# Optimization experiments

Measured on AMD Instinct MI355X. Metric: run time of the kernel, lower is better.

Reference implementation:

```python
import jax, jax.numpy as jnp
import numpy as np

HID = 2048
N_HEADS = 16
N_KV = 16
HEAD_DIM = HID // N_HEADS
N_EXP = 8
TOP_K = 2
MOE_I = 1408
SH_I = 5632
EPS = 1e-6
ROPE_THETA = 1e6


def _rms(x, w):
    v = jnp.mean(jnp.square(x), axis=-1, keepdims=True)
    return (x * jax.lax.rsqrt(v + EPS)) * w


def _rope(q, k):
    # q, k: [B, S, H, D]
    S, D = q.shape[1], q.shape[-1]
    inv = 1.0 / (ROPE_THETA ** (jnp.arange(0, D, 2, dtype=jnp.float32) / D))
    freqs = jnp.arange(S, dtype=jnp.float32)[:, None] * inv[None, :]   # [S, D/2]
    emb = jnp.concatenate([freqs, freqs], axis=-1)                      # [S, D]
    cos = jnp.cos(emb)[None, :, None, :]
    sin = jnp.sin(emb)[None, :, None, :]
    def rot(t):
        t1, t2 = t[..., : D // 2], t[..., D // 2:]
        return jnp.concatenate([-t2, t1], axis=-1)
    return q * cos + rot(q) * sin, k * cos + rot(k) * sin


def setup_inputs() -> dict:
    key = jax.random.key(0)
    ks = jax.random.split(key, 20)
    s = 0.02
    d = {
        "x": jax.random.normal(ks[0], (2, 1024, HID), jnp.float32),
        "w_ln1": jnp.ones((HID,), jnp.float32),
        "wq": jax.random.normal(ks[1], (HID, N_HEADS * HEAD_DIM), jnp.float32) * s,
        "bq": jnp.zeros((N_HEADS * HEAD_DIM,), jnp.float32),
        "wk": jax.random.normal(ks[2], (HID, N_KV * HEAD_DIM), jnp.float32) * s,
        "bk": jnp.zeros((N_KV * HEAD_DIM,), jnp.float32),
        "wv": jax.random.normal(ks[3], (HID, N_KV * HEAD_DIM), jnp.float32) * s,
        "bv": jnp.zeros((N_KV * HEAD_DIM,), jnp.float32),
        "wo": jax.random.normal(ks[4], (N_HEADS * HEAD_DIM, HID), jnp.float32) * s,
        "w_ln2": jnp.ones((HID,), jnp.float32),
        "w_router": jax.random.normal(ks[5], (HID, N_EXP), jnp.float32) * s,
        "w_gate_e": jax.random.normal(ks[6], (N_EXP, HID, MOE_I), jnp.float32) * s,
        "w_up_e": jax.random.normal(ks[7], (N_EXP, HID, MOE_I), jnp.float32) * s,
        "w_down_e": jax.random.normal(ks[8], (N_EXP, MOE_I, HID), jnp.float32) * s,
        "w_sh_gate": jax.random.normal(ks[9], (HID, SH_I), jnp.float32) * s,
        "w_sh_up": jax.random.normal(ks[10], (HID, SH_I), jnp.float32) * s,
        "w_sh_down": jax.random.normal(ks[11], (SH_I, HID), jnp.float32) * s,
        "w_sh_eg": jax.random.normal(ks[12], (HID, 1), jnp.float32) * s,
    }
    return d


def reference(x, w_ln1, wq, bq, wk, bk, wv, bv, wo, w_ln2, w_router,
              w_gate_e, w_up_e, w_down_e, w_sh_gate, w_sh_up, w_sh_down, w_sh_eg):
    B, S, H = x.shape
    # ---- self-attention (pre-norm) ----
    h = _rms(x, w_ln1)
    q = (h @ wq + bq).reshape(B, S, N_HEADS, HEAD_DIM)
    k = (h @ wk + bk).reshape(B, S, N_KV, HEAD_DIM)
    v = (h @ wv + bv).reshape(B, S, N_KV, HEAD_DIM)
    q, k = _rope(q, k)
    rep = N_HEADS // N_KV
    if rep > 1:
        k = jnp.repeat(k, rep, axis=2)
        v = jnp.repeat(v, rep, axis=2)
    scores = jnp.einsum("bqhd,bkhd->bhqk", q, k) * (HEAD_DIM ** -0.5)
    causal = jnp.tril(jnp.ones((S, S), bool))
    scores = jnp.where(causal[None, None], scores, jnp.finfo(scores.dtype).min)
    attn = jax.nn.softmax(scores, axis=-1)
    ctx = jnp.einsum("bhqk,bkhd->bqhd", attn, v).reshape(B, S, N_HEADS * HEAD_DIM)
    x = x + ctx @ wo

    # ---- sparse MoE FFN (pre-norm) ----
    h = _rms(x, w_ln2).reshape(B * S, H)                     # [T, H]
    logits = h @ w_router                                     # [T, E]
    probs = jax.nn.softmax(logits, axis=-1)
    top_w, top_i = jax.lax.top_k(probs, TOP_K)               # norm_topk_prob=False
    combine = jnp.sum(jax.nn.one_hot(top_i, N_EXP, dtype=h.dtype)
                      * top_w[..., None], axis=1)            # [T, E]
    # dense per-expert compute combined with routing weights (same math as
    # the sorted grouped-GEMM dispatch in Qwen2MoeMLPStack)
    g = jnp.einsum("th,ehi->eti", h, w_gate_e)               # [E, T, I]
    u = jnp.einsum("th,ehi->eti", h, w_up_e)
    y = jnp.einsum("eti,eih->eth", jax.nn.silu(g) * u, w_down_e)
    routed = jnp.einsum("eth,te->th", y, combine)            # [T, H]
    # shared expert with sigmoid gate
    sh = (jax.nn.silu(h @ w_sh_gate) * (h @ w_sh_up)) @ w_sh_down
    sh = sh * jax.nn.sigmoid(h @ w_sh_eg)
    x = x + (routed + sh).reshape(B, S, H)
    return x
```

## Files before the change

kernel.cpp:

```cpp
#include <hip/hip_runtime.h>
#include <hip/hip_bf16.h>
#include <math.h>

#define TOKENS 2048
#define HIDDEN 2048
#define NH 16
#define HD 128
#define SEQ 1024
#define MOE_I 1408
#define SH_I 5632
#define K3 6144
#define MAXROWS 5120

typedef __hip_bfloat16 bf16;
typedef short bf16x8 __attribute__((ext_vector_type(8)));
typedef short bf16x4 __attribute__((ext_vector_type(4)));
typedef float f32x4 __attribute__((ext_vector_type(4)));

__device__ __forceinline__ float b2f(bf16 x) { return __bfloat162float(x); }
__device__ __forceinline__ bf16 f2b(float x) { return __float2bfloat16(x); }
__device__ __forceinline__ void split2(float v, short& hi, short& lo) {
    bf16 h = f2b(v);
    bf16 l = f2b(v - b2f(h));
    hi = __builtin_bit_cast(short, h); lo = __builtin_bit_cast(short, l);
}

__device__ __forceinline__ void load_lds16(const void* g, void* l) {
    __builtin_amdgcn_global_load_lds(
        (const __attribute__((address_space(1))) unsigned int*)g,
        (__attribute__((address_space(3))) unsigned int*)l, 16, 0, 0);
}

__global__ __launch_bounds__(256) void rmsnorm3_k(
    const float* __restrict__ x, const float* __restrict__ w, bf16* __restrict__ out)
{
    const int row = blockIdx.x, tid = threadIdx.x;
    const float4* xr = (const float4*)(x + (size_t)row * HIDDEN);
    float4 v1 = xr[tid], v2 = xr[tid + 256];
    float ss = v1.x*v1.x + v1.y*v1.y + v1.z*v1.z + v1.w*v1.w
             + v2.x*v2.x + v2.y*v2.y + v2.z*v2.z + v2.w*v2.w;
    #pragma unroll
    for (int off = 1; off < 64; off <<= 1) ss += __shfl_xor(ss, off);
    __shared__ float ps[4];
    if ((tid & 63) == 0) ps[tid >> 6] = ss;
    __syncthreads();
    float tot = ps[0] + ps[1] + ps[2] + ps[3];
    float r = rsqrtf(tot * (1.0f / HIDDEN) + 1e-6f);
    bf16* o = out + (size_t)row * 4096;
    float vv[8] = {v1.x, v1.y, v1.z, v1.w, v2.x, v2.y, v2.z, v2.w};
    int idx[8]  = {tid*4, tid*4+1, tid*4+2, tid*4+3,
                   1024+tid*4, 1024+tid*4+1, 1024+tid*4+2, 1024+tid*4+3};
    #pragma unroll
    for (int u = 0; u < 8; u++) {
        short hi, lo; split2(vv[u] * r * w[idx[u]], hi, lo);
        o[idx[u]]        = __builtin_bit_cast(bf16, hi);
        o[2048 + idx[u]] = __builtin_bit_cast(bf16, lo);
    }
}

__global__ __launch_bounds__(256) void transpose_wz(
    const float* __restrict__ W, bf16* __restrict__ Wt, int K, int N,
    int nOff, long zsrc, long zdst)
{
    __shared__ float t[32][33];
    W  += (size_t)blockIdx.z * zsrc;
    Wt += (size_t)blockIdx.z * zdst;
    const int n0 = blockIdx.x * 32, k0 = blockIdx.y * 32;
    const int tx = threadIdx.x & 31, ty = threadIdx.x >> 5;
    #pragma unroll
    for (int i = 0; i < 4; i++)
        t[ty + i*8][tx] = W[(size_t)(k0 + ty + i*8) * N + n0 + tx];
    __syncthreads();
    #pragma unroll
    for (int i = 0; i < 4; i++)
        Wt[(size_t)(nOff + n0 + ty + i*8) * K + k0 + tx] = f2b(t[tx][ty + i*8]);
}

__global__ __launch_bounds__(256) void transpose_w3(
    const float* __restrict__ W, bf16* __restrict__ Wt2, int K, int N, int nOff)
{
    __shared__ float t[32][33];
    const int n0 = blockIdx.x * 32, k0 = blockIdx.y * 32;
    const int tx = threadIdx.x & 31, ty = threadIdx.x >> 5;
    #pragma unroll
    for (int i = 0; i < 4; i++)
        t[ty + i*8][tx] = W[(size_t)(k0 + ty + i*8) * N + n0 + tx];
    __syncthreads();
    #pragma unroll
    for (int i = 0; i < 4; i++) {
        float v = t[tx][ty + i*8];
        short hi, lo; split2(v, hi, lo);
        bf16* o = Wt2 + (size_t)(nOff + n0 + ty + i*8) * (2*K) + k0 + tx;
        o[0] = __builtin_bit_cast(bf16, hi);
        o[K] = __builtin_bit_cast(bf16, lo);
    }
}

__global__ __launch_bounds__(256) void gemm_bt(
    const bf16* __restrict__ A, const bf16* __restrict__ Bt,
    float* __restrict__ Cf, bf16* __restrict__ Cb, const float* __restrict__ bias,
    int M, int N, int K, int ldA, int ldB, int ldC, long zCstride, int limb3, int epi)
{
    __shared__ __align__(16) bf16 As[128 * 32];
    __shared__ __align__(16) bf16 Bs[128 * 32];
    const int tid = threadIdx.x;
    const int lane = tid & 63, wid = tid >> 6;
    const int l16 = lane & 15, lh = lane >> 4;
    const int wr = wid >> 1, wc = wid & 1;
    const int m0 = blockIdx.x * 128, n0 = blockIdx.y * 128;
    const int f = tid * 8;
    const int r0 = f >> 5, c0 = f & 31;
    const int koff = blockIdx.z * K;

    f32x4 acc[4][4];
    #pragma unroll
    for (int m = 0; m < 4; m++)
        #pragma unroll
        for (int n = 0; n < 4; n++) acc[m][n] = (f32x4){0.f, 0.f, 0.f, 0.f};

    const bf16* Ag0 = A + (size_t)(m0 + r0) * ldA + c0;
    const bf16* Ag1 = Ag0 + (size_t)64 * ldA;
    const bf16* Bg0 = Bt + (size_t)(n0 + r0) * ldB + c0;
    const bf16* Bg1 = Bg0 + (size_t)64 * ldB;

    for (int k0 = 0; k0 < K; k0 += 32) {
        const int kcat = koff + k0;
        int ka = kcat, kb = kcat;
        if (limb3) {
            ka = (kcat >= 4096) ? kcat - 4096 : kcat;
            kb = (kcat >= 2048) ? kcat - 2048 : kcat;
        }
        __syncthreads();
        load_lds16(Ag0 + ka, As + f);
        load_lds16(Ag1 + ka, As + f + 2048);
        load_lds16(Bg0 + kb, Bs + f);
        load_lds16(Bg1 + kb, Bs + f + 2048);
        __syncthreads();
        bf16x8 a[4], b[4];
        #pragma unroll
        for (int m = 0; m < 4; m++)
            a[m] = *(const bf16x8*)&As[(wr*64 + m*16 + l16) * 32 + lh*8];
        #pragma unroll
        for (int n = 0; n < 4; n++)
            b[n] = *(const bf16x8*)&Bs[(wc*64 + n*16 + l16) * 32 + lh*8];
        #pragma unroll
        for (int m = 0; m < 4; m++)
            #pragma unroll
            for (int n = 0; n < 4; n++)
                acc[m][n] = __builtin_amdgcn_mfma_f32_16x16x32_bf16(a[m], b[n], acc[m][n], 0, 0, 0);
    }

    float* Cz = Cf + (size_t)blockIdx.z * zCstride;
    #pragma unroll
    for (int m = 0; m < 4; m++) {
        const int grow_base = m0 + wr*64 + m*16 + lh*4;
        #pragma unroll
        for (int n = 0; n < 4; n++) {
            const int gcol = n0 + wc*64 + n*16 + l16;
            #pragma unroll
            for (int j = 0; j < 4; j++) {
                const size_t o = (size_t)(grow_base + j) * ldC + gcol;
                const float v = acc[m][n][j];
                if (epi == 0)      Cb[o] = f2b(v);
                else if (epi == 4) Cz[o] = v;
                else               Cf[o] = v + bias[gcol];
            }
        }
    }
}

__global__ __launch_bounds__(256) void gemm_gu(
    const bf16* __restrict__ A, const bf16* __restrict__ BtAll,
    const int* __restrict__ offc, const int* __restrict__ perm,
    bf16* __restrict__ C)
{
    const int e = blockIdx.z;
    const int off = offc[8 + e];
    const int padCnt = offc[9 + e] - off;
    const int m0 = blockIdx.x * 128;
    if (m0 >= padCnt) return;
    __shared__ __align__(16) bf16 As[128 * 32];
    __shared__ __align__(16) bf16 Bs[128 * 32];
    const int tid = threadIdx.x;
    const int lane = tid & 63, wid = tid >> 6;
    const int l16 = lane & 15, lh = lane >> 4;
    const int wr = wid >> 1, wc = wid & 1;
    const int n0 = blockIdx.y * 128;
    const int f = tid * 8;
    const int r0 = f >> 5, c0 = f & 31;
    const bf16* Bt = BtAll + (size_t)e * 2816 * 2048;

    int t0 = perm[off + m0 + r0];      if (t0 < 0) t0 = 0;
    int t1 = perm[off + m0 + r0 + 64]; if (t1 < 0) t1 = 0;

    f32x4 acc[4][4];
    #pragma unroll
    for (int m = 0; m < 4; m++)
        #pragma unroll
        for (int n = 0; n < 4; n++) acc[m][n] = (f32x4){0.f, 0.f, 0.f, 0.f};

    const bf16* Ag0 = A + (size_t)t0 * 2048 + c0;
    const bf16* Ag1 = A + (size_t)t1 * 2048 + c0;
    const bf16* Bg0 = Bt + (size_t)(n0 + r0) * 2048 + c0;
    const bf16* Bg1 = Bg0 + (size_t)64 * 2048;

    for (int k0 = 0; k0 < 2048; k0 += 32) {
        __syncthreads();
        load_lds16(Ag0 + k0, As + f);
        load_lds16(Ag1 + k0, As + f + 2048);
        load_lds16(Bg0 + k0, Bs + f);
        load_lds16(Bg1 + k0, Bs + f + 2048);
        __syncthreads();
        bf16x8 a[4], b[4];
        #pragma unroll
        for (int m = 0; m < 4; m++)
            a[m] = *(const bf16x8*)&As[(wr*64 + m*16 + l16) * 32 + lh*8];
        #pragma unroll
        for (int n = 0; n < 4; n++)
            b[n] = *(const bf16x8*)&Bs[(wc*64 + n*16 + l16) * 32 + lh*8];
        #pragma unroll
        for (int m = 0; m < 4; m++)
            #pragma unroll
            for (int n = 0; n < 4; n++)
                acc[m][n] = __builtin_amdgcn_mfma_f32_16x16x32_bf16(a[m], b[n], acc[m][n], 0, 0, 0);
    }

    #pragma unroll
    for (int m = 0; m < 4; m++) {
        const int grow_base = m0 + wr*64 + m*16 + lh*4;
        #pragma unroll
        for (int n = 0; n < 4; n++) {
            const int gcol = n0 + wc*64 + n*16 + l16;
            #pragma unroll
            for (int j = 0; j < 4; j++)
                C[(size_t)(off + grow_base + j) * 2816 + gcol] = f2b(acc[m][n][j]);
        }
    }
}

__global__ __launch_bounds__(256) void gemm_down(
    const bf16* __restrict__ A, const bf16* __restrict__ BtAll,
    const int* __restrict__ offc, bf16* __restrict__ Y)
{
    const int e = blockIdx.z;
    const int off = offc[8 + e];
    const int padCnt = offc[9 + e] - off;
    const int m0 = blockIdx.x * 128;
    if (m0 >= padCnt) return;
    __shared__ __align__(16) bf16 As[128 * 32];
    __shared__ __align__(16) bf16 Bs[128 * 32];
    const int tid = threadIdx.x;
    const int lane = tid & 63, wid = tid >> 6;
    const int l16 = lane & 15, lh = lane >> 4;
    const int wr = wid >> 1, wc = wid & 1;
    const int n0 = blockIdx.y * 128;
    const int f = tid * 8;
    const int r0 = f >> 5, c0 = f & 31;
    const bf16* Bt = BtAll + (size_t)e * 2048 * 1408;

    f32x4 acc[4][4];
    #pragma unroll
    for (int m = 0; m < 4; m++)
        #pragma unroll
        for (int n = 0; n < 4; n++) acc[m][n] = (f32x4){0.f, 0.f, 0.f, 0.f};

    const bf16* Ag0 = A + (size_t)(off + m0 + r0) * 1408 + c0;
    const bf16* Ag1 = Ag0 + (size_t)64 * 1408;
    const bf16* Bg0 = Bt + (size_t)(n0 + r0) * 1408 + c0;
    const bf16* Bg1 = Bg0 + (size_t)64 * 1408;

    for (int k0 = 0; k0 < 1408; k0 += 32) {
        __syncthreads();
        load_lds16(Ag0 + k0, As + f);
        load_lds16(Ag1 + k0, As + f + 2048);
        load_lds16(Bg0 + k0, Bs + f);
        load_lds16(Bg1 + k0, Bs + f + 2048);
        __syncthreads();
        bf16x8 a[4], b[4];
        #pragma unroll
        for (int m = 0; m < 4; m++)
            a[m] = *(const bf16x8*)&As[(wr*64 + m*16 + l16) * 32 + lh*8];
        #pragma unroll
        for (int n = 0; n < 4; n++)
            b[n] = *(const bf16x8*)&Bs[(wc*64 + n*16 + l16) * 32 + lh*8];
        #pragma unroll
        for (int m = 0; m < 4; m++)
            #pragma unroll
            for (int n = 0; n < 4; n++)
                acc[m][n] = __builtin_amdgcn_mfma_f32_16x16x32_bf16(a[m], b[n], acc[m][n], 0, 0, 0);
    }

    #pragma unroll
    for (int m = 0; m < 4; m++) {
        const int grow_base = m0 + wr*64 + m*16 + lh*4;
        #pragma unroll
        for (int n = 0; n < 4; n++) {
            const int gcol = n0 + wc*64 + n*16 + l16;
            #pragma unroll
            for (int j = 0; j < 4; j++)
                Y[(size_t)(off + grow_base + j) * 2048 + gcol] = f2b(acc[m][n][j]);
        }
    }
}

__global__ void rope_f32_k(float* __restrict__ qkv)
{
    const int idx = blockIdx.x * 256 + threadIdx.x;
    const int d  = idx & 63;
    const int hh = (idx >> 6) & 15;
    const size_t base = (size_t)(idx >> 10) * 6144 + hh * HD;
    const int s = (idx >> 10) & 1023;
    const float fr = (float)s * powf(1.0e6f, -(float)d * (1.0f / 64.0f));
    float c, sn;
    sincosf(fr, &sn, &c);
    float q0 = qkv[base + d], q1 = qkv[base + d + 64];
    qkv[base + d]      = q0 * c - q1 * sn;
    qkv[base + d + 64] = q1 * c + q0 * sn;
    float k0 = qkv[base + 2048 + d], k1 = qkv[base + 2048 + d + 64];
    qkv[base + 2048 + d]      = k0 * c - k1 * sn;
    qkv[base + 2048 + d + 64] = k1 * c + k0 * sn;
}

__global__ __launch_bounds__(256) void transpose_v3_k(
    const float* __restrict__ qkv, bf16* __restrict__ vth, bf16* __restrict__ vtl)
{
    __shared__ float t[32][33];
    const int s0 = blockIdx.x * 32, d0 = blockIdx.y * 32;
    const int bh = blockIdx.z, b = bh >> 4, h = bh & 15;
    const int tx = threadIdx.x & 31, ty = threadIdx.x >> 5;
    const float* vb = qkv + ((size_t)b * SEQ) * 6144 + 4096 + h * HD;
    #pragma unroll
    for (int i = 0; i < 4; i++)
        t[ty + i*8][tx] = vb[(size_t)(s0 + ty + i*8) * 6144 + d0 + tx];
    __syncthreads();
    const size_t ob = ((size_t)bh * HD) * SEQ;
    #pragma unroll
    for (int i = 0; i < 4; i++) {
        float val = t[tx][ty + i*8];
        short hi, lo; split2(val, hi, lo);
        const size_t o = ob + (size_t)(d0 + ty + i*8) * SEQ + s0 + tx;
        vth[o] = __builtin_bit_cast(bf16, hi);
        vtl[o] = __builtin_bit_cast(bf16, lo);
    }
}

__global__ __launch_bounds__(256) void attn3_k(
    const float* __restrict__ qkv,
    const bf16* __restrict__ vth, const bf16* __restrict__ vtl,
    bf16* __restrict__ ctx2)
{
    __shared__ __align__(16) bf16 Ksh[32 * 128], Ksl[32 * 128];
    __shared__ __align__(16) bf16 Vth[128 * 32], Vtl[128 * 32];
    __shared__ __align__(16) bf16 Ph[4][16 * 32], Pl[4][16 * 32];
    const int tid = threadIdx.x, lane = tid & 63, wid = tid >> 6;
    const int l16 = lane & 15, lh = lane >> 4;
    const int bh = blockIdx.y, b = bh >> 4, h = bh & 15;
    const int qbase = blockIdx.x * 64;
    const int qw = qbase + wid * 16;
    const float* qp = qkv + ((size_t)b * SEQ) * 6144 + h * HD;
    const float* kp = qkv + ((size_t)b * SEQ) * 6144 + 2048 + h * HD;
    const bf16* vph = vth + ((size_t)bh * HD) * SEQ;
    const bf16* vpl = vtl + ((size_t)bh * HD) * SEQ;

    bf16x8 aqh[4], aql[4];
    #pragma unroll
    for (int c = 0; c < 4; c++) {
        const float* qrow = qp + (size_t)(qw + l16) * 6144 + c*32 + lh*8;
        #pragma unroll
        for (int u = 0; u < 8; u++) {
            short hi, lo; split2(qrow[u], hi, lo);
            aqh[c][u] = hi; aql[c][u] = lo;
        }
    }

    f32x4 o[8];
    #pragma unroll
    for (int n = 0; n < 8; n++) o[n] = (f32x4){0.f, 0.f, 0.f, 0.f};
    float mj[4], lj[4];
    #pragma unroll
    for (int j = 0; j < 4; j++) { mj[j] = -1e30f; lj[j] = 0.f; }

    const int f = tid * 8;
    const int kr = tid >> 3, kc = (tid & 7) * 16;
    const int kt_end = qbase / 32 + 2;
    for (int kt = 0; kt < kt_end; ++kt) {
        const int kv0 = kt * 32;
        __syncthreads();
        {
            const float* krow = kp + (size_t)(kv0 + kr) * 6144 + kc;
            #pragma unroll
            for (int u = 0; u < 4; u++) {
                float4 kv4 = *(const float4*)(krow + u*4);
                short h0, l0, h1, l1, h2s, l2s, h3, l3;
                split2(kv4.x, h0, l0); split2(kv4.y, h1, l1);
                split2(kv4.z, h2s, l2s); split2(kv4.w, h3, l3);
                bf16x4 h4, l4;
                h4[0] = h0; h4[1] = h1; h4[2] = h2s; h4[3] = h3;
                l4[0] = l0; l4[1] = l1; l4[2] = l2s; l4[3] = l3;
                *(bf16x4*)&Ksh[kr*128 + kc + u*4] = h4;
                *(bf16x4*)&Ksl[kr*128 + kc + u*4] = l4;
            }
        }
        load_lds16(vph + (size_t)(f >> 5) * SEQ + kv0 + (f & 31), Vth + f);
        load_lds16(vph + (size_t)((f >> 5) + 64) * SEQ + kv0 + (f & 31), Vth + f + 2048);
        load_lds16(vpl + (size_t)(f >> 5) * SEQ + kv0 + (f & 31), Vtl + f);
        load_lds16(vpl + (size_t)((f >> 5) + 64) * SEQ + kv0 + (f & 31), Vtl + f + 2048);
        __syncthreads();

        f32x4 s0a = (f32x4){0.f,0.f,0.f,0.f}, s1a = (f32x4){0.f,0.f,0.f,0.f};
        #pragma unroll
        for (int c = 0; c < 4; c++) {
            bf16x8 bk0h = *(const bf16x8*)&Ksh[(l16) * 128 + c*32 + lh*8];
            bf16x8 bk0l = *(const bf16x8*)&Ksl[(l16) * 128 + c*32 + lh*8];
            bf16x8 bk1h = *(const bf16x8*)&Ksh[(l16 + 16) * 128 + c*32 + lh*8];
            bf16x8 bk1l = *(const bf16x8*)&Ksl[(l16 + 16) * 128 + c*32 + lh*8];
            s0a = __builtin_amdgcn_mfma_f32_16x16x32_bf16(aqh[c], bk0h, s0a, 0, 0, 0);
            s0a = __builtin_amdgcn_mfma_f32_16x16x32_bf16(aql[c], bk0h, s0a, 0, 0, 0);
            s0a = __builtin_amdgcn_mfma_f32_16x16x32_bf16(aqh[c], bk0l, s0a, 0, 0, 0);
            s1a = __builtin_amdgcn_mfma_f32_16x16x32_bf16(aqh[c], bk1h, s1a, 0, 0, 0);
            s1a = __builtin_amdgcn_mfma_f32_16x16x32_bf16(aql[c], bk1h, s1a, 0, 0, 0);
            s1a = __builtin_amdgcn_mfma_f32_16x16x32_bf16(aqh[c], bk1l, s1a, 0, 0, 0);
        }
        const float scale = 0.08838834764831845f;
        #pragma unroll
        for (int j = 0; j < 4; j++) {
            const int qrow = qw + lh*4 + j;
            float s0 = s0a[j] * scale, s1 = s1a[j] * scale;
            if (kv0 + l16 > qrow)      s0 = -1e30f;
            if (kv0 + l16 + 16 > qrow) s1 = -1e30f;
            float mx = fmaxf(s0, s1);
            #pragma unroll
            for (int off = 1; off < 16; off <<= 1) mx = fmaxf(mx, __shfl_xor(mx, off, 16));
            const float nm = fmaxf(mj[j], mx);
            const float al = __expf(mj[j] - nm);
            const float p0 = __expf(s0 - nm), p1 = __expf(s1 - nm);
            float rs = p0 + p1;
            #pragma unroll
            for (int off = 1; off < 16; off <<= 1) rs += __shfl_xor(rs, off, 16);
            lj[j] = lj[j] * al + rs;
            mj[j] = nm;
            #pragma unroll
            for (int n = 0; n < 8; n++) o[n][j] *= al;
            short h0, l0, h1, l1;
            split2(p0, h0, l0); split2(p1, h1, l1);
            Ph[wid][(lh*4 + j) * 32 + l16]      = __builtin_bit_cast(bf16, h0);
            Pl[wid][(lh*4 + j) * 32 + l16]      = __builtin_bit_cast(bf16, l0);
            Ph[wid][(lh*4 + j) * 32 + l16 + 16] = __builtin_bit_cast(bf16, h1);
            Pl[wid][(lh*4 + j) * 32 + l16 + 16] = __builtin_bit_cast(bf16, l1);
        }
        __syncthreads();
        const bf16x8 aph = *(const bf16x8*)&Ph[wid][l16 * 32 + lh*8];
        const bf16x8 apl = *(const bf16x8*)&Pl[wid][l16 * 32 + lh*8];
        #pragma unroll
        for (int n = 0; n < 8; n++) {
            bf16x8 bvh = *(const bf16x8*)&Vth[(n*16 + l16) * 32 + lh*8];
            bf16x8 bvl = *(const bf16x8*)&Vtl[(n*16 + l16) * 32 + lh*8];
            o[n] = __builtin_amdgcn_mfma_f32_16x16x32_bf16(aph, bvh, o[n], 0, 0, 0);
            o[n] = __builtin_amdgcn_mfma_f32_16x16x32_bf16(apl, bvh, o[n], 0, 0, 0);
            o[n] = __builtin_amdgcn_mfma_f32_16x16x32_bf16(aph, bvl, o[n], 0, 0, 0);
        }
    }

    float inv[4];
    #pragma unroll
    for (int j = 0; j < 4; j++) inv[j] = 1.0f / lj[j];
    #pragma unroll
    for (int n = 0; n < 8; n++)
        #pragma unroll
        for (int j = 0; j < 4; j++) {
            const float v = o[n][j] * inv[j];
            short hi, lo; split2(v, hi, lo);
            const size_t base = ((size_t)b * SEQ + (qw + lh*4 + j)) * 4096 + h * HD + n*16 + l16;
            ctx2[base]        = __builtin_bit_cast(bf16, hi);
            ctx2[base + 2048] = __builtin_bit_cast(bf16, lo);
        }
}

__global__ __launch_bounds__(256) void combine_rms_k(
    const float* __restrict__ x, const float* __restrict__ xp,
    const float* __restrict__ w, float* __restrict__ x1, bf16* __restrict__ h2)
{
    const int row = blockIdx.x, tid = threadIdx.x;
    const size_t rb = (size_t)row * HIDDEN;
    const long zs = (long)TOKENS * HIDDEN;
    float4 v[2];
    #pragma unroll
    for (int u = 0; u < 2; u++) {
        const int i = tid + u * 256;
        float4 a  = ((const float4*)(x + rb))[i];
        float4 p0 = ((const float4*)(xp + rb))[i];
        float4 p1 = ((const float4*)(xp + zs + rb))[i];
        float4 p2 = ((const float4*)(xp + 2*zs + rb))[i];
        v[u].x = a.x + p0.x + p1.x + p2.x;
        v[u].y = a.y + p0.y + p1.y + p2.y;
        v[u].z = a.z + p0.z + p1.z + p2.z;
        v[u].w = a.w + p0.w + p1.w + p2.w;
        ((float4*)(x1 + rb))[i] = v[u];
    }
    float ss = v[0].x*v[0].x + v[0].y*v[0].y + v[0].z*v[0].z + v[0].w*v[0].w
             + v[1].x*v[1].x + v[1].y*v[1].y + v[1].z*v[1].z + v[1].w*v[1].w;
    #pragma unroll
    for (int off = 1; off < 64; off <<= 1) ss += __shfl_xor(ss, off);
    __shared__ float ps[4];
    if ((tid & 63) == 0) ps[tid >> 6] = ss;
    __syncthreads();
    float tot = ps[0] + ps[1] + ps[2] + ps[3];
    float r = rsqrtf(tot * (1.0f / HIDDEN) + 1e-6f);
    #pragma unroll
    for (int u = 0; u < 2; u++) {
        const int i = (tid + u * 256) * 4;
        h2[rb + i]     = f2b(v[u].x * r * w[i]);
        h2[rb + i + 1] = f2b(v[u].y * r * w[i+1]);
        h2[rb + i + 2] = f2b(v[u].z * r * w[i+2]);
        h2[rb + i + 3] = f2b(v[u].w * r * w[i+3]);
    }
}

__global__ __launch_bounds__(256) void router_k(
    const float* __restrict__ x1, const float* __restrict__ wln,
    const float* __restrict__ wr, const float* __restrict__ weg,
    float* __restrict__ combine, float* __restrict__ sigeg)
{
    const int wid = threadIdx.x >> 6, lane = threadIdx.x & 63;
    const int t = blockIdx.x * 4 + wid;
    const float* xr = x1 + (size_t)t * HIDDEN;
    float ss = 0.f;
    for (int c = lane; c < HIDDEN; c += 64) { const float v = xr[c]; ss += v * v; }
    #pragma unroll
    for (int off = 1; off < 64; off <<= 1) ss += __shfl_xor(ss, off);
    const float r = rsqrtf(ss * (1.0f / HIDDEN) + 1e-6f);

    float acc[9];
    #pragma unroll
    for (int e = 0; e < 9; e++) acc[e] = 0.f;
    for (int c = lane; c < HIDDEN; c += 64) {
        const float hv = xr[c] * r * wln[c];
        const float* wrow = wr + (size_t)c * 8;
        #pragma unroll
        for (int e = 0; e < 8; e++) acc[e] += hv * wrow[e];
        acc[8] += hv * weg[c];
    }
    #pragma unroll
    for (int e = 0; e < 9; e++)
        #pragma unroll
        for (int off = 1; off < 64; off <<= 1) acc[e] += __shfl_xor(acc[e], off);
    float mx = acc[0];
    #pragma unroll
    for (int e = 1; e < 8; e++) mx = fmaxf(mx, acc[e]);
    float p[8], s = 0.f;
    #pragma unroll
    for (int e = 0; e < 8; e++) { p[e] = expf(acc[e] - mx); s += p[e]; }
    const float invs = 1.0f / s;
    #pragma unroll
    for (int e = 0; e < 8; e++) p[e] *= invs;
    int i1 = 0;
    #pragma unroll
    for (int e = 1; e < 8; e++) if (p[e] > p[i1]) i1 = e;
    int i2 = (i1 == 0) ? 1 : 0;
    #pragma unroll
    for (int e = 0; e < 8; e++) if (e != i1 && p[e] > p[i2]) i2 = e;
    if (lane < 8) combine[(size_t)t * 8 + lane] = (lane == i1 || lane == i2) ? p[lane] : 0.f;
    if (lane == 0) sigeg[t] = 1.0f / (1.0f + expf(-acc[8]));
}

__global__ __launch_bounds__(256) void count_fill_k(
    const float* __restrict__ comb, int* __restrict__ offc, int* __restrict__ perm,
    float* __restrict__ scale, int* __restrict__ inv)
{
    __shared__ int cnt[8], off[9], fil[8];
    const int tid = threadIdx.x;
    if (tid < 8) { cnt[tid] = 0; fil[tid] = 0; }
    __syncthreads();
    for (int t = tid; t < TOKENS; t += 256)
        #pragma unroll
        for (int e = 0; e < 8; e++)
            if (comb[(size_t)t * 8 + e] > 0.f) atomicAdd(&cnt[e], 1);
    __syncthreads();
    if (tid == 0) {
        off[0] = 0;
        for (int e = 0; e < 8; e++) off[e+1] = off[e] + ((cnt[e] + 127) & ~127);
    }
    __syncthreads();
    for (int i = tid; i < MAXROWS; i += 256) { perm[i] = -1; scale[i] = 0.f; }
    __syncthreads();
    for (int t = tid; t < TOKENS; t += 256) {
        int j = 0;
        #pragma unroll
        for (int e = 0; e < 8; e++) {
            const float c = comb[(size_t)t * 8 + e];
            if (c > 0.f) {
                int s = atomicAdd(&fil[e], 1);
                int slot = off[e] + s;
                perm[slot] = t;
                scale[slot] = c;
                inv[t * 2 + j] = slot;
                j++;
            }
        }
    }
    __syncthreads();
    if (tid < 9) offc[8 + tid] = off[tid];
}

__global__ void silu_k(const bf16* __restrict__ g, bf16* __restrict__ a,
                       const float* __restrict__ rowScale,
                       int I, int ldg, int rowsConst, const int* __restrict__ rowsPtr)
{
    const int idx = (blockIdx.x * 256 + threadIdx.x) * 4;
    const int rows = rowsPtr ? *rowsPtr : rowsConst;
    const int row = idx / I;
    if (row >= rows) return;
    const int col = idx - row * I;
    const float s = rowScale[row];
    const bf16* gr = g + (size_t)row * ldg + col;
    bf16* ar = a + (size_t)row * I + col;
    #pragma unroll
    for (int c = 0; c < 4; c++) {
        const float gv = b2f(gr[c]), uv = b2f(gr[I + c]);
        ar[c] = f2b(s * gv / (1.0f + __expf(-gv)) * uv);
    }
}

__global__ void final_k(const float* __restrict__ x1, const bf16* __restrict__ y,
                        const int* __restrict__ inv, const float* __restrict__ ysh,
                        float* __restrict__ out)
{
    const int i = blockIdx.x * 256 + threadIdx.x;
    const int t = i >> 9;
    const int col = (i & 511) * 4;
    const int s0 = inv[t*2], s1 = inv[t*2 + 1];
    const long zs = (long)TOKENS * HIDDEN;
    float4 a  = ((const float4*)x1)[i];
    float4 h0 = ((const float4*)ysh)[i];
    float4 h1 = ((const float4*)(ysh + zs))[i];
    const bf16* y0 = y + (size_t)s0 * 2048 + col;
    const bf16* y1 = y + (size_t)s1 * 2048 + col;
    float4 r;
    r.x = a.x + h0.x + h1.x + b2f(y0[0]) + b2f(y1[0]);
    r.y = a.y + h0.y + h1.y + b2f(y0[1]) + b2f(y1[1]);
    r.z = a.z + h0.z + h1.z + b2f(y0[2]) + b2f(y1[2]);
    r.w = a.w + h0.w + h1.w + b2f(y0[3]) + b2f(y1[3]);
    ((float4*)out)[i] = r;
}

extern "C" void kernel_launch(void* const* d_in, const int* in_sizes, int n_in,
                              void* d_out, int out_size, void* d_ws, size_t ws_size,
                              hipStream_t stream)
{
    const float* x     = (const float*)d_in[0];
    const float* w_ln1 = (const float*)d_in[1];
    const float* wq    = (const float*)d_in[2];
    const float* bq    = (const float*)d_in[3];
    const float* wk    = (const float*)d_in[4];
    const float* bk    = (const float*)d_in[5];
    const float* wv    = (const float*)d_in[6];
    const float* bv    = (const float*)d_in[7];
    const float* wo    = (const float*)d_in[8];
    const float* w_ln2 = (const float*)d_in[9];
    const float* w_rt  = (const float*)d_in[10];
    const float* w_ge  = (const float*)d_in[11];
    const float* w_ue  = (const float*)d_in[12];
    const float* w_de  = (const float*)d_in[13];
    const float* w_sg  = (const float*)d_in[14];
    const float* w_su  = (const float*)d_in[15];
    const float* w_sd  = (const float*)d_in[16];
    const float* w_eg  = (const float*)d_in[17];
    float* out = (float*)d_out;
    (void)in_sizes; (void)n_in; (void)out_size; (void)ws_size;

    char* ws = (char*)d_ws;
    float* x1    = (float*)(ws + 0);
    bf16*  h2    = (bf16*)(ws + 16777216);
    float* comb  = (float*)(ws + 25165824);
    float* seg   = (float*)(ws + 25231360);
    int*   offc  = (int*)(ws + 25239552);
    float* scale = (float*)(ws + 25243648);
    int*   perm  = (int*)(ws + 25276416);
    int*   inv   = (int*)(ws + 25297920);
    float* bqkv  = (float*)(ws + 25314304);
    const size_t S = 25341952;
    bf16*  hcat  = (bf16*)(ws + S);
    bf16*  wtqkv = (bf16*)(ws + S + 16777216);
    float* qkvf  = (float*)(ws + S + 67108864);
    bf16*  vth   = (bf16*)(ws + S);
    bf16*  vtl   = (bf16*)(ws + S + 8388608);
    bf16*  ctx2  = (bf16*)(ws + S + 16777216);
    bf16*  wt3o  = (bf16*)(ws + S + 33554432);
    float* xp    = (float*)(ws + S + 50331648);
    bf16*  wtgu  = (bf16*)(ws + S);
    bf16*  gb    = (bf16*)(ws + S + 92274688);
    bf16*  ab    = (bf16*)(ws + S);
    bf16*  wtd   = (bf16*)(ws + S + 14417920);
    bf16*  ymoe  = (bf16*)(ws + S + 60555264);
    bf16*  wtshgu = (bf16*)(ws + S);
    bf16*  gsh    = (bf16*)(ws + S + 81526784);
    bf16*  ash    = (bf16*)(ws + S);
    bf16*  wtshd  = (bf16*)(ws + S + 23068672);
    float* ysh    = (float*)(ws + S + 81526784);

    rmsnorm3_k<<<TOKENS, 256, 0, stream>>>(x, w_ln1, hcat);
    (void)hipMemcpyAsync(bqkv,        bq, 8192, hipMemcpyDeviceToDevice, stream);
    (void)hipMemcpyAsync(bqkv + 2048, bk, 8192, hipMemcpyDeviceToDevice, stream);
    (void)hipMemcpyAsync(bqkv + 4096, bv, 8192, hipMemcpyDeviceToDevice, stream);

    transpose_w3<<<dim3(64, 64), 256, 0, stream>>>(wq, wtqkv, HIDDEN, HIDDEN, 0);
    transpose_w3<<<dim3(64, 64), 256, 0, stream>>>(wk, wtqkv, HIDDEN, HIDDEN, 2048);
    transpose_w3<<<dim3(64, 64), 256, 0, stream>>>(wv, wtqkv, HIDDEN, HIDDEN, 4096);
    gemm_bt<<<dim3(16, 48, 1), 256, 0, stream>>>(hcat, wtqkv, qkvf, nullptr, bqkv,
                                                 TOKENS, 6144, K3, 4096, 4096, 6144, 0, 1, 5);

    rope_f32_k<<<8192, 256, 0, stream>>>(qkvf);
    transpose_v3_k<<<dim3(32, 4, 32), 256, 0, stream>>>(qkvf, vth, vtl);
    attn3_k<<<dim3(16, 32), 256, 0, stream>>>(qkvf, vth, vtl, ctx2);

    transpose_w3<<<dim3(64, 64), 256, 0, stream>>>(wo, wt3o, HIDDEN, HIDDEN, 0);
    gemm_bt<<<dim3(16, 16, 3), 256, 0, stream>>>(ctx2, wt3o, xp, nullptr, nullptr,
                                                 TOKENS, HIDDEN, 2048, 4096, 4096, 2048,
                                                 (long)TOKENS * HIDDEN, 1, 4);
    combine_rms_k<<<TOKENS, 256, 0, stream>>>(x, xp, w_ln2, x1, h2);

    router_k<<<TOKENS / 4, 256, 0, stream>>>(x1, w_ln2, w_rt, w_eg, comb, seg);
    count_fill_k<<<1, 256, 0, stream>>>(comb, offc, perm, scale, inv);

    transpose_wz<<<dim3(44, 64, 8), 256, 0, stream>>>(w_ge, wtgu, HIDDEN, MOE_I, 0,
                                                      (long)HIDDEN*MOE_I, (long)2816*HIDDEN);
    transpose_wz<<<dim3(44, 64, 8), 256, 0, stream>>>(w_ue, wtgu, HIDDEN, MOE_I, MOE_I,
                                                      (long)HIDDEN*MOE_I, (long)2816*HIDDEN);
    gemm_gu<<<dim3(MAXROWS/128, 22, 8), 256, 0, stream>>>(h2, wtgu, offc, perm, gb);
    silu_k<<<(MAXROWS * MOE_I) / 1024, 256, 0, stream>>>(gb, ab, scale, MOE_I, 2816, 0, offc + 16);
    transpose_wz<<<dim3(64, 44, 8), 256, 0, stream>>>(w_de, wtd, MOE_I, HIDDEN, 0,
                                                      (long)MOE_I*HIDDEN, (long)HIDDEN*MOE_I);
    gemm_down<<<dim3(MAXROWS/128, 16, 8), 256, 0, stream>>>(ab, wtd, offc, ymoe);

    transpose_wz<<<dim3(176, 64, 1), 256, 0, stream>>>(w_sg, wtshgu, HIDDEN, SH_I, 0, 0, 0);
    transpose_wz<<<dim3(176, 64, 1), 256, 0, stream>>>(w_su, wtshgu, HIDDEN, SH_I, SH_I, 0, 0);
    gemm_bt<<<dim3(16, 88, 1), 256, 0, stream>>>(h2, wtshgu, nullptr, gsh, nullptr,
                                                 TOKENS, 2*SH_I, HIDDEN, HIDDEN, HIDDEN, 2*SH_I, 0, 0, 0);
    silu_k<<<(TOKENS * SH_I) / 1024, 256, 0, stream>>>(gsh, ash, seg, SH_I, 2*SH_I, TOKENS, nullptr);
    transpose_wz<<<dim3(64, 176, 1), 256, 0, stream>>>(w_sd, wtshd, SH_I, HIDDEN, 0, 0, 0);
    gemm_bt<<<dim3(16, 16, 2), 256, 0, stream>>>(ash, wtshd, ysh, nullptr, nullptr,
                                                 TOKENS, HIDDEN, SH_I/2, SH_I, SH_I, 2048,
                                                 (long)TOKENS * HIDDEN, 0, 4);

    final_k<<<(TOKENS * HIDDEN) / 1024, 256, 0, stream>>>(x1, ymoe, inv, ysh, out);
}
```

Baseline: 1.167 ms.

## Use 32x32 MFMA in GEMMs, XCD-aware block remap, precompute RoPE table

After: 1.155 ms. Within noise of the previous version (-1.0%).

```diff
diff --git a/kernel.cpp b/kernel.cpp
--- a/kernel.cpp
+++ b/kernel.cpp
@@ -16,6 +16,7 @@
 typedef short bf16x8 __attribute__((ext_vector_type(8)));
 typedef short bf16x4 __attribute__((ext_vector_type(4)));
 typedef float f32x4 __attribute__((ext_vector_type(4)));
+typedef float f32x16 __attribute__((ext_vector_type(16)));
 
 __device__ __forceinline__ float b2f(bf16 x) { return __bfloat162float(x); }
 __device__ __forceinline__ bf16 f2b(float x) { return __float2bfloat16(x); }
@@ -105,18 +106,27 @@
     __shared__ __align__(16) bf16 Bs[128 * 32];
     const int tid = threadIdx.x;
     const int lane = tid & 63, wid = tid >> 6;
-    const int l16 = lane & 15, lh = lane >> 4;
+    const int l32 = lane & 31, lh2 = lane >> 5;
     const int wr = wid >> 1, wc = wid & 1;
-    const int m0 = blockIdx.x * 128, n0 = blockIdx.y * 128;
+    int lid = blockIdx.y * gridDim.x + blockIdx.x;
+    {
+        const int nwg = gridDim.x * gridDim.y;
+        const int q = nwg >> 3, r = nwg & 7;
+        const int xcd = lid & 7, idx = lid >> 3;
+        lid = (xcd < r ? xcd * (q + 1) : r * (q + 1) + (xcd - r) * q) + idx;
+    }
+    const int m0 = (lid % gridDim.x) * 128, n0 = (lid / gridDim.x) * 128;
     const int f = tid * 8;
     const int r0 = f >> 5, c0 = f & 31;
     const int koff = blockIdx.z * K;
 
-    f32x4 acc[4][4];
-    #pragma unroll
-    for (int m = 0; m < 4; m++)
-        #pragma unroll
-        for (int n = 0; n < 4; n++) acc[m][n] = (f32x4){0.f, 0.f, 0.f, 0.f};
+    f32x16 acc[2][2];
+    #pragma unroll
+    for (int m = 0; m < 2; m++)
+        #pragma unroll
+        for (int n = 0; n < 2; n++)
+            #pragma unroll
+            for (int j = 0; j < 16; j++) acc[m][n][j] = 0.f;
 
     const bf16* Ag0 = A + (size_t)(m0 + r0) * ldA + c0;
     const bf16* Ag1 = Ag0 + (size_t)64 * ldA;
@@ -136,31 +146,38 @@
         load_lds16(Bg0 + kb, Bs + f);
         load_lds16(Bg1 + kb, Bs + f + 2048);
         __syncthreads();
-        bf16x8 a[4], b[4];
-        #pragma unroll
-        for (int m = 0; m < 4; m++)
-            a[m] = *(const bf16x8*)&As[(wr*64 + m*16 + l16) * 32 + lh*8];
-        #pragma unroll
-        for (int n = 0; n < 4; n++)
-            b[n] = *(const bf16x8*)&Bs[(wc*64 + n*16 + l16) * 32 + lh*8];
-        #pragma unroll
-        for (int m = 0; m < 4; m++)
-            #pragma unroll
-            for (int n = 0; n < 4; n++)
-                acc[m][n] = __builtin_amdgcn_mfma_f32_16x16x32_bf16(a[m], b[n], acc[m][n], 0, 0, 0);
+        bf16x8 a[2][2], b[2][2];
+        #pragma unroll
+        for (int m = 0; m < 2; m++)
+            #pragma unroll
+            for (int kk = 0; kk < 2; kk++)
+                a[m][kk] = *(const bf16x8*)&As[(wr*64 + m*32 + l32) * 32 + kk*16 + lh2*8];
+        #pragma unroll
+        for (int n = 0; n < 2; n++)
+            #pragma unroll
+            for (int kk = 0; kk < 2; kk++)
+                b[n][kk] = *(const bf16x8*)&Bs[(wc*64 + n*32 + l32) * 32 + kk*16 + lh2*8];
+        #pragma unroll
+        for (int m = 0; m < 2; m++)
+            #pragma unroll
+            for (int n = 0; n < 2; n++)
+                #pragma unroll
+                for (int kk = 0; kk < 2; kk++)
+                    acc[m][n] = __builtin_amdgcn_mfma_f32_32x32x16_bf16(a[m][kk], b[n][kk], acc[m][n], 0, 0, 0);
     }
 
     float* Cz = Cf + (size_t)blockIdx.z * zCstride;
     #pragma unroll
-    for (int m = 0; m < 4; m++) {
-        const int grow_base = m0 + wr*64 + m*16 + lh*4;
-        #pragma unroll
-        for (int n = 0; n < 4; n++) {
-            const int gcol = n0 + wc*64 + n*16 + l16;
-            #pragma unroll
-            for (int j = 0; j < 4; j++) {
-                const size_t o = (size_t)(grow_base + j) * ldC + gcol;
-                const float v = acc[m][n][j];
+    for (int m = 0; m < 2; m++) {
+        const int base_m = m0 + wr*64 + m*32 + 4*lh2;
+        #pragma unroll
+        for (int n = 0; n < 2; n++) {
+            const int gcol = n0 + wc*64 + n*32 + l32;
+            #pragma unroll
+            for (int reg = 0; reg < 16; reg++) {
+                const int grow = base_m + (reg & 3) + 8*(reg >> 2);
+                const size_t o = (size_t)grow * ldC + gcol;
+                const float v = acc[m][n][reg];
                 if (epi == 0)      Cb[o] = f2b(v);
                 else if (epi == 4) Cz[o] = v;
                 else               Cf[o] = v + bias[gcol];
@@ -183,7 +200,7 @@
     __shared__ __align__(16) bf16 Bs[128 * 32];
     const int tid = threadIdx.x;
     const int lane = tid & 63, wid = tid >> 6;
-    const int l16 = lane & 15, lh = lane >> 4;
+    const int l32 = lane & 31, lh2 = lane >> 5;
     const int wr = wid >> 1, wc = wid & 1;
     const int n0 = blockIdx.y * 128;
     const int f = tid * 8;
@@ -193,11 +210,13 @@
     int t0 = perm[off + m0 + r0];      if (t0 < 0) t0 = 0;
     int t1 = perm[off + m0 + r0 + 64]; if (t1 < 0) t1 = 0;
 
-    f32x4 acc[4][4];
-    #pragma unroll
-    for (int m = 0; m < 4; m++)
-        #pragma unroll
-        for (int n = 0; n < 4; n++) acc[m][n] = (f32x4){0.f, 0.f, 0.f, 0.f};
+    f32x16 acc[2][2];
+    #pragma unroll
+    for (int m = 0; m < 2; m++)
+        #pragma unroll
+        for (int n = 0; n < 2; n++)
+            #pragma unroll
+            for (int j = 0; j < 16; j++) acc[m][n][j] = 0.f;
 
     const bf16* Ag0 = A + (size_t)t0 * 2048 + c0;
     const bf16* Ag1 = A + (size_t)t1 * 2048 + c0;
@@ -211,29 +230,37 @@
         load_lds16(Bg0 + k0, Bs + f);
         load_lds16(Bg1 + k0, Bs + f + 2048);
         __syncthreads();
-        bf16x8 a[4], b[4];
-        #pragma unroll
-        for (int m = 0; m < 4; m++)
-            a[m] = *(const bf16x8*)&As[(wr*64 + m*16 + l16) * 32 + lh*8];
-        #pragma unroll
-        for (int n = 0; n < 4; n++)
-            b[n] = *(const bf16x8*)&Bs[(wc*64 + n*16 + l16) * 32 + lh*8];
-        #pragma unroll
-        for (int m = 0; m < 4; m++)
-            #pragma unroll
-            for (int n = 0; n < 4; n++)
-                acc[m][n] = __builtin_amdgcn_mfma_f32_16x16x32_bf16(a[m], b[n], acc[m][n], 0, 0, 0);
-    }
-
-    #pragma unroll
-    for (int m = 0; m < 4; m++) {
-        const int grow_base = m0 + wr*64 + m*16 + lh*4;
-        #pragma unroll
-        for (int n = 0; n < 4; n++) {
-            const int gcol = n0 + wc*64 + n*16 + l16;
-            #pragma unroll
-            for (int j = 0; j < 4; j++)
-                C[(size_t)(off + grow_base + j) * 2816 + gcol] = f2b(acc[m][n][j]);
+        bf16x8 a[2][2], b[2][2];
+        #pragma unroll
+        for (int m = 0; m < 2; m++)
+            #pragma unroll
+            for (int kk = 0; kk < 2; kk++)
+                a[m][kk] = *(const bf16x8*)&As[(wr*64 + m*32 + l32) * 32 + kk*16 + lh2*8];
+        #pragma unroll
+        for (int n = 0; n < 2; n++)
+            #pragma unroll
+            for (int kk = 0; kk < 2; kk++)
+                b[n][kk] = *(const bf16x8*)&Bs[(wc*64 + n*32 + l32) * 32 + kk*16 + lh2*8];
+        #pragma unroll
+        for (int m = 0; m < 2; m++)
+            #pragma unroll
+            for (int n = 0; n < 2; n++)
+                #pragma unroll
+                for (int kk = 0; kk < 2; kk++)
+                    acc[m][n] = __builtin_amdgcn_mfma_f32_32x32x16_bf16(a[m][kk], b[n][kk], acc[m][n], 0, 0, 0);
+    }
+
+    #pragma unroll
+    for (int m = 0; m < 2; m++) {
+        const int base_m = m0 + wr*64 + m*32 + 4*lh2;
+        #pragma unroll
+        for (int n = 0; n < 2; n++) {
+            const int gcol = n0 + wc*64 + n*32 + l32;
+            #pragma unroll
+            for (int reg = 0; reg < 16; reg++) {
+                const int grow = base_m + (reg & 3) + 8*(reg >> 2);
+                C[(size_t)(off + grow) * 2816 + gcol] = f2b(acc[m][n][reg]);
+            }
         }
     }
 }
@@ -251,18 +278,20 @@
     __shared__ __align__(16) bf16 Bs[128 * 32];
     const int tid = threadIdx.x;
     const int lane = tid & 63, wid = tid >> 6;
-    const int l16 = lane & 15, lh = lane >> 4;
+    const int l32 = lane & 31, lh2 = lane >> 5;
     const int wr = wid >> 1, wc = wid & 1;
     const int n0 = blockIdx.y * 128;
     const int f = tid * 8;
     const int r0 = f >> 5, c0 = f & 31;
     const bf16* Bt = BtAll + (size_t)e * 2048 * 1408;
 
-    f32x4 acc[4][4];
-    #pragma unroll
-    for (int m = 0; m < 4; m++)
-        #pragma unroll
-        for (int n = 0; n < 4; n++) acc[m][n] = (f32x4){0.f, 0.f, 0.f, 0.f};
+    f32x16 acc[2][2];
+    #pragma unroll
+    for (int m = 0; m < 2; m++)
+        #pragma unroll
+        for (int n = 0; n < 2; n++)
+            #pragma unroll
+            for (int j = 0; j < 16; j++) acc[m][n][j] = 0.f;
 
     const bf16* Ag0 = A + (size_t)(off + m0 + r0) * 1408 + c0;
     const bf16* Ag1 = Ag0 + (size_t)64 * 1408;
@@ -276,43 +305,60 @@
         load_lds16(Bg0 + k0, Bs + f);
         load_lds16(Bg1 + k0, Bs + f + 2048);
         __syncthreads();
-        bf16x8 a[4], b[4];
-        #pragma unroll
-        for (int m = 0; m < 4; m++)
-            a[m] = *(const bf16x8*)&As[(wr*64 + m*16 + l16) * 32 + lh*8];
-        #pragma unroll
-        for (int n = 0; n < 4; n++)
-            b[n] = *(const bf16x8*)&Bs[(wc*64 + n*16 + l16) * 32 + lh*8];
-        #pragma unroll
-        for (int m = 0; m < 4; m++)
-            #pragma unroll
-            for (int n = 0; n < 4; n++)
-                acc[m][n] = __builtin_amdgcn_mfma_f32_16x16x32_bf16(a[m], b[n], acc[m][n], 0, 0, 0);
-    }
-
-    #pragma unroll
-    for (int m = 0; m < 4; m++) {
-        const int grow_base = m0 + wr*64 + m*16 + lh*4;
-        #pragma unroll
-        for (int n = 0; n < 4; n++) {
-            const int gcol = n0 + wc*64 + n*16 + l16;
-            #pragma unroll
-            for (int j = 0; j < 4; j++)
-                Y[(size_t)(off + grow_base + j) * 2048 + gcol] = f2b(acc[m][n][j]);
-        }
-    }
-}
-
-__global__ void rope_f32_k(float* __restrict__ qkv)
+        bf16x8 a[2][2], b[2][2];
+        #pragma unroll
+        for (int m = 0; m < 2; m++)
+            #pragma unroll
+            for (int kk = 0; kk < 2; kk++)
+                a[m][kk] = *(const bf16x8*)&As[(wr*64 + m*32 + l32) * 32 + kk*16 + lh2*8];
+        #pragma unroll
+        for (int n = 0; n < 2; n++)
+            #pragma unroll
+            for (int kk = 0; kk < 2; kk++)
+                b[n][kk] = *(const bf16x8*)&Bs[(wc*64 + n*32 + l32) * 32 + kk*16 + lh2*8];
+        #pragma unroll
+        for (int m = 0; m < 2; m++)
+            #pragma unroll
+            for (int n = 0; n < 2; n++)
+                #pragma unroll
+                for (int kk = 0; kk < 2; kk++)
+                    acc[m][n] = __builtin_amdgcn_mfma_f32_32x32x16_bf16(a[m][kk], b[n][kk], acc[m][n], 0, 0, 0);
+    }
+
+    #pragma unroll
+    for (int m = 0; m < 2; m++) {
+        const int base_m = m0 + wr*64 + m*32 + 4*lh2;
+        #pragma unroll
+        for (int n = 0; n < 2; n++) {
+            const int gcol = n0 + wc*64 + n*32 + l32;
+            #pragma unroll
+            for (int reg = 0; reg < 16; reg++) {
+                const int grow = base_m + (reg & 3) + 8*(reg >> 2);
+                Y[(size_t)(off + grow) * 2048 + gcol] = f2b(acc[m][n][reg]);
+            }
+        }
+    }
+}
+
+__global__ void rope_table_k(float2* __restrict__ cs)
+{
+    const int i = blockIdx.x * 256 + threadIdx.x;
+    const int s = i >> 6, d = i & 63;
+    const float fr = (float)s * powf(1.0e6f, -(float)d * (1.0f / 64.0f));
+    float c, sn;
+    sincosf(fr, &sn, &c);
+    cs[i] = make_float2(c, sn);
+}
+
+__global__ void rope_f32_k(float* __restrict__ qkv, const float2* __restrict__ cs)
 {
     const int idx = blockIdx.x * 256 + threadIdx.x;
     const int d  = idx & 63;
     const int hh = (idx >> 6) & 15;
     const size_t base = (size_t)(idx >> 10) * 6144 + hh * HD;
     const int s = (idx >> 10) & 1023;
-    const float fr = (float)s * powf(1.0e6f, -(float)d * (1.0f / 64.0f));
-    float c, sn;
-    sincosf(fr, &sn, &c);
+    const float2 t = cs[(s << 6) | d];
+    const float c = t.x, sn = t.y;
     float q0 = qkv[base + d], q1 = qkv[base + d + 64];
     qkv[base + d]      = q0 * c - q1 * sn;
     qkv[base + d + 64] = q1 * c + q0 * sn;
@@ -678,7 +724,8 @@
     int*   perm  = (int*)(ws + 25276416);
     int*   inv   = (int*)(ws + 25297920);
     float* bqkv  = (float*)(ws + 25314304);
-    const size_t S = 25341952;
+    float2* ropecs = (float2*)(ws + 25338880);
+    const size_t S = 25863168;
     bf16*  hcat  = (bf16*)(ws + S);
     bf16*  wtqkv = (bf16*)(ws + S + 16777216);
     float* qkvf  = (float*)(ws + S + 67108864);
@@ -702,6 +749,7 @@
     (void)hipMemcpyAsync(bqkv,        bq, 8192, hipMemcpyDeviceToDevice, stream);
     (void)hipMemcpyAsync(bqkv + 2048, bk, 8192, hipMemcpyDeviceToDevice, stream);
     (void)hipMemcpyAsync(bqkv + 4096, bv, 8192, hipMemcpyDeviceToDevice, stream);
+    rope_table_k<<<256, 256, 0, stream>>>(ropecs);
 
     transpose_w3<<<dim3(64, 64), 256, 0, stream>>>(wq, wtqkv, HIDDEN, HIDDEN, 0);
     transpose_w3<<<dim3(64, 64), 256, 0, stream>>>(wk, wtqkv, HIDDEN, HIDDEN, 2048);
@@ -709,7 +757,7 @@
     gemm_bt<<<dim3(16, 48, 1), 256, 0, stream>>>(hcat, wtqkv, qkvf, nullptr, bqkv,
                                                  TOKENS, 6144, K3, 4096, 4096, 6144, 0, 1, 5);
 
-    rope_f32_k<<<8192, 256, 0, stream>>>(qkvf);
+    rope_f32_k<<<8192, 256, 0, stream>>>(qkvf, ropecs);
     transpose_v3_k<<<dim3(32, 4, 32), 256, 0, stream>>>(qkvf, vth, vtl);
     attn3_k<<<dim3(16, 32), 256, 0, stream>>>(qkvf, vth, vtl, ctx2);
 
```
